# Kernel optimization log

Measured on AMD Instinct MI355X. Metric: run time of the kernel, lower is better.

## Reference

```python
import jax, jax.numpy as jnp
import numpy as np

N = 6144       # number of nodes (adj_list[0].shape[0])
NFEAT = 512    # in_dim
NHID = 256     # hid_dim
NCLASS = 8     # out_dim
ADIM = 128     # attention_dim
EPS = 1e-9


def setup_inputs() -> dict:
    key = jax.random.key(0)
    ks = jax.random.split(key, 16)
    rn = lambda k, s, sc=0.05: (jax.random.normal(k, s, dtype=jnp.float32) * sc)
    return {
        # three dense adjacency matrices (non-negative, largely dense surrogate)
        "adj0": jax.random.uniform(ks[0], (N, N), dtype=jnp.float32),
        "adj1": jax.random.uniform(ks[1], (N, N), dtype=jnp.float32),
        "adj2": jax.random.uniform(ks[2], (N, N), dtype=jnp.float32),
        "features": jax.random.normal(ks[3], (N, NFEAT), dtype=jnp.float32),
        # atten / atten2 / atten3 : Linear(N -> ADIM)
        "Wa1": rn(ks[4], (N, ADIM)), "ba1": jnp.zeros((ADIM,), jnp.float32),
        "Wa2": rn(ks[5], (N, ADIM)), "ba2": jnp.zeros((ADIM,), jnp.float32),
        "Wa3": rn(ks[6], (N, ADIM)), "ba3": jnp.zeros((ADIM,), jnp.float32),
        # agg : Linear(3*ADIM -> 3)
        "Wagg": rn(ks[7], (3 * ADIM, 3)), "bagg": jnp.zeros((3,), jnp.float32),
        # gcn1 : GraphConvolution(NFEAT -> NHID)
        "W1": rn(ks[8], (NFEAT, NHID)), "b1": jnp.zeros((NHID,), jnp.float32),
        # Q/K/V : Linear(NHID -> NHID)
        "Wq": rn(ks[9], (NHID, NHID)), "bq": jnp.zeros((NHID,), jnp.float32),
        "Wk": rn(ks[10], (NHID, NHID)), "bk": jnp.zeros((NHID,), jnp.float32),
        "Wv": rn(ks[11], (NHID, NHID)), "bv": jnp.zeros((NHID,), jnp.float32),
        # gcn2 : GraphConvolution(NHID -> NCLASS)
        "W2": rn(ks[12], (NHID, NCLASS)), "b2": jnp.zeros((NCLASS,), jnp.float32),
    }


def _gcn_norm(a):
    # symmetric normalization D^{-1/2} A D^{-1/2}
    d = jnp.sum(a, axis=1)
    dinv = jnp.where(d > 0, jax.lax.rsqrt(d + EPS), 0.0)
    return dinv[:, None] * a * dinv[None, :]


def reference(adj0, adj1, adj2, features,
              Wa1, ba1, Wa2, ba2, Wa3, ba3, Wagg, bagg,
              W1, b1, Wq, bq, Wk, bk, Wv, bv, W2, b2):
    # adjacency attention weights
    z1 = adj0 @ Wa1 + ba1                      # [N, ADIM]
    z2 = adj1 @ Wa2 + ba2
    z3 = adj2 @ Wa3 + ba3
    z4 = jnp.concatenate((z1, z2, z3), axis=1) @ Wagg + bagg   # [N, 3]
    nz = jax.nn.softmax(z4, axis=1)
    # torch broadcasting: nz[:, i] (shape [N]) scales COLUMNS of adj_i
    adj = nz[:, 0] * adj0 + nz[:, 1] * adj1 + nz[:, 2] * adj2  # [N, N]
    # gcn1
    x = jax.nn.relu(adj @ (features @ W1) + b1)                # [N, NHID]
    Q_h = x @ Wq + bq
    K_h = x @ Wk + bk
    V_h = x @ Wv + bv
    # adjacency-masked dense attention
    A_tilde = adj * (Q_h @ K_h.T)                              # [N, N]
    attention = jax.nn.softmax(A_tilde, axis=1)
    X_tilde = jax.nn.relu(_gcn_norm(attention) @ V_h)          # [N, NHID]
    # gcn2
    z = adj @ (X_tilde @ W2) + b2                              # [N, NCLASS]
    return jax.nn.softmax(z, axis=1), nz
```

## Files before the change

kernel.cpp:

```cpp
#include <hip/hip_runtime.h>

#define NN 6144
#define NF 512
#define NH 256
#define AD 128
#define NC 8

typedef short bf16x8 __attribute__((ext_vector_type(8)));
typedef float f32x4 __attribute__((ext_vector_type(4)));

__device__ __forceinline__ float4 ld4(const float* p) {
    return *reinterpret_cast<const float4*>(p);
}
__device__ __forceinline__ void st4(float* p, float4 v) {
    *reinterpret_cast<float4*>(p) = v;
}

__device__ __forceinline__ f32x4 mfma16(bf16x8 a, bf16x8 b, f32x4 c) {
    return __builtin_amdgcn_mfma_f32_16x16x32_bf16(a, b, c, 0, 0, 0);
}

__device__ __forceinline__ void async_copy16(const void* g, void* lds) {
    __builtin_amdgcn_global_load_lds(
        (const __attribute__((address_space(1))) void*)g,
        (__attribute__((address_space(3))) void*)lds, 16, 0, 0);
}

__device__ __forceinline__ void split1(float f, ushort& h, ushort& l) {
    unsigned u = __float_as_uint(f);
    unsigned hr = (u + 0x7FFFu + ((u >> 16) & 1u)) >> 16;
    float fh = __uint_as_float(hr << 16);
    float fl = f - fh;
    unsigned ul = __float_as_uint(fl);
    unsigned lr = (ul + 0x7FFFu + ((ul >> 16) & 1u)) >> 16;
    h = (ushort)hr; l = (ushort)lr;
}

__global__ __launch_bounds__(256) void k0_prep(
    const float* __restrict__ Wa1, const float* __restrict__ Wa2, const float* __restrict__ Wa3,
    const float* __restrict__ ba1, const float* __restrict__ ba2, const float* __restrict__ ba3,
    const float* __restrict__ Wagg, const float* __restrict__ bagg,
    float* __restrict__ U, float* __restrict__ cvec)
{
    int idx = blockIdx.x * 256 + threadIdx.x;
    if (idx < 3 * NN * 3) {
        int i = idx / (NN * 3);
        int rem = idx - i * (NN * 3);
        int r = rem / 3, j = rem - 3 * (rem / 3);
        const float* Wa = (i == 0) ? Wa1 : ((i == 1) ? Wa2 : Wa3);
        float s = 0.f;
        #pragma unroll 4
        for (int k = 0; k < AD; ++k)
            s += Wa[(size_t)r * AD + k] * Wagg[(i * AD + k) * 3 + j];
        U[idx] = s;
    }
    if (blockIdx.x == 0 && threadIdx.x < 3) {
        int j = threadIdx.x;
        float s = bagg[j];
        const float* bas[3] = {ba1, ba2, ba3};
        for (int i = 0; i < 3; ++i)
            for (int k = 0; k < AD; ++k)
                s += bas[i][k] * Wagg[(i * AD + k) * 3 + j];
        cvec[j] = s;
    }
}

__global__ __launch_bounds__(256) void k1_nz(
    const float* __restrict__ adj0, const float* __restrict__ adj1, const float* __restrict__ adj2,
    const float* __restrict__ U, const float* __restrict__ cvec,
    float* __restrict__ nzT, float* __restrict__ out_nz)
{
    int r0 = blockIdx.x * 4;
    int tid = threadIdx.x;
    float acc[4][3] = {};
    for (int c = tid; c < NN; c += 256) {
        float u[3][3];
        #pragma unroll
        for (int i = 0; i < 3; ++i) {
            u[i][0] = U[((size_t)i * NN + c) * 3 + 0];
            u[i][1] = U[((size_t)i * NN + c) * 3 + 1];
            u[i][2] = U[((size_t)i * NN + c) * 3 + 2];
        }
        #pragma unroll
        for (int rr = 0; rr < 4; ++rr) {
            size_t off = (size_t)(r0 + rr) * NN + c;
            float a0 = adj0[off], a1 = adj1[off], a2 = adj2[off];
            acc[rr][0] += a0 * u[0][0] + a1 * u[1][0] + a2 * u[2][0];
            acc[rr][1] += a0 * u[0][1] + a1 * u[1][1] + a2 * u[2][1];
            acc[rr][2] += a0 * u[0][2] + a1 * u[1][2] + a2 * u[2][2];
        }
    }
    __shared__ float red[256][12];
    #pragma unroll
    for (int rr = 0; rr < 4; ++rr)
        #pragma unroll
        for (int j = 0; j < 3; ++j)
            red[tid][rr * 3 + j] = acc[rr][j];
    __syncthreads();
    for (int s = 128; s > 0; s >>= 1) {
        if (tid < s) {
            #pragma unroll
            for (int q = 0; q < 12; ++q) red[tid][q] += red[tid + s][q];
        }
        __syncthreads();
    }
    if (tid < 4) {
        int r = r0 + tid;
        float z0 = red[0][tid * 3 + 0] + cvec[0];
        float z1 = red[0][tid * 3 + 1] + cvec[1];
        float z2 = red[0][tid * 3 + 2] + cvec[2];
        float m = fmaxf(z0, fmaxf(z1, z2));
        float e0 = __expf(z0 - m), e1 = __expf(z1 - m), e2 = __expf(z2 - m);
        float inv = 1.f / (e0 + e1 + e2);
        e0 *= inv; e1 *= inv; e2 *= inv;
        nzT[0 * NN + r] = e0; nzT[1 * NN + r] = e1; nzT[2 * NN + r] = e2;
        out_nz[(size_t)r * 3 + 0] = e0;
        out_nz[(size_t)r * 3 + 1] = e1;
        out_nz[(size_t)r * 3 + 2] = e2;
    }
}

__global__ __launch_bounds__(256) void k2_adj(
    const float* __restrict__ adj0, const float* __restrict__ adj1, const float* __restrict__ adj2,
    const float* __restrict__ nzT, float* __restrict__ adj)
{
    size_t idx = (size_t)blockIdx.x * 256 + threadIdx.x;
    size_t e = idx * 4;
    int c = (int)(e % NN);
    float4 a0 = ld4(adj0 + e), a1 = ld4(adj1 + e), a2 = ld4(adj2 + e);
    float4 w0 = ld4(nzT + c), w1 = ld4(nzT + NN + c), w2 = ld4(nzT + 2 * NN + c);
    float4 o;
    o.x = w0.x * a0.x + w1.x * a1.x + w2.x * a2.x;
    o.y = w0.y * a0.y + w1.y * a1.y + w2.y * a2.y;
    o.z = w0.z * a0.z + w1.z * a1.z + w2.z * a2.z;
    o.w = w0.w * a0.w + w1.w * a1.w + w2.w * a2.w;
    st4(adj + e, o);
}

#define BM 64
#define BN 64
#define BK 32
#define ASTR 68

__global__ __launch_bounds__(256) void gemm64(
    const float* __restrict__ A, int lda,
    const float* __restrict__ B, int ldb,
    float* __restrict__ C, int ldc,
    int Kdim, const float* __restrict__ bias, int relu)
{
    __shared__ float As[BK * ASTR];
    __shared__ float Bs[BK * BN];
    int tid = threadIdx.x;
    int tm = tid >> 4, tn = tid & 15;
    int rowBase = blockIdx.y * BM, colBase = blockIdx.x * BN;
    float acc[4][4] = {};
    for (int k0 = 0; k0 < Kdim; k0 += BK) {
        #pragma unroll
        for (int it = 0; it < 2; ++it) {
            int lin = it * 256 + tid;
            int am = lin >> 3, ak4 = lin & 7;
            float4 a = ld4(A + (size_t)(rowBase + am) * lda + k0 + ak4 * 4);
            int kk = ak4 * 4;
            As[(kk + 0) * ASTR + am] = a.x;
            As[(kk + 1) * ASTR + am] = a.y;
            As[(kk + 2) * ASTR + am] = a.z;
            As[(kk + 3) * ASTR + am] = a.w;
        }
        #pragma unroll
        for (int it = 0; it < 2; ++it) {
            int lin = it * 256 + tid;
            int bk = lin >> 4, bn4 = lin & 15;
            float4 b = ld4(B + (size_t)(k0 + bk) * ldb + colBase + bn4 * 4);
            st4(&Bs[bk * BN + bn4 * 4], b);
        }
        __syncthreads();
        #pragma unroll
        for (int k = 0; k < BK; ++k) {
            float4 av = *reinterpret_cast<const float4*>(&As[k * ASTR + tm * 4]);
            float4 bv = *reinterpret_cast<const float4*>(&Bs[k * BN + tn * 4]);
            float am_[4] = {av.x, av.y, av.z, av.w};
            float bn_[4] = {bv.x, bv.y, bv.z, bv.w};
            #pragma unroll
            for (int i = 0; i < 4; ++i)
                #pragma unroll
                for (int j = 0; j < 4; ++j)
                    acc[i][j] += am_[i] * bn_[j];
        }
        __syncthreads();
    }
    #pragma unroll
    for (int i = 0; i < 4; ++i) {
        int row = rowBase + tm * 4 + i;
        int col = colBase + tn * 4;
        float4 o = {acc[i][0], acc[i][1], acc[i][2], acc[i][3]};
        if (bias) {
            o.x += bias[col]; o.y += bias[col + 1];
            o.z += bias[col + 2]; o.w += bias[col + 3];
        }
        if (relu) {
            o.x = fmaxf(o.x, 0.f); o.y = fmaxf(o.y, 0.f);
            o.z = fmaxf(o.z, 0.f); o.w = fmaxf(o.w, 0.f);
        }
        st4(C + (size_t)row * ldc + col, o);
    }
}

__global__ __launch_bounds__(256) void cvt_hl(
    const float* __restrict__ in, ushort* __restrict__ hi, ushort* __restrict__ lo)
{
    size_t base = ((size_t)blockIdx.x * 256 + threadIdx.x) * 4;
    float4 v = ld4(in + base);
    ushort4 h, l;
    split1(v.x, h.x, l.x); split1(v.y, h.y, l.y);
    split1(v.z, h.z, l.z); split1(v.w, h.w, l.w);
    *reinterpret_cast<ushort4*>(hi + base) = h;
    *reinterpret_cast<ushort4*>(lo + base) = l;
}

__global__ __launch_bounds__(256) void cvt_t(
    const float* __restrict__ in, int R, int C,
    ushort* __restrict__ outhi, ushort* __restrict__ outlo)
{
    __shared__ float t[32][33];
    int rb = blockIdx.x * 32, cb = blockIdx.y * 32;
    int tid = threadIdx.x;
    int lr = tid >> 3, lc4 = (tid & 7) * 4;
    float4 v = ld4(in + (size_t)(rb + lr) * C + cb + lc4);
    t[lr][lc4 + 0] = v.x; t[lr][lc4 + 1] = v.y;
    t[lr][lc4 + 2] = v.z; t[lr][lc4 + 3] = v.w;
    __syncthreads();
    ushort4 h, l;
    split1(t[lc4 + 0][lr], h.x, l.x);
    split1(t[lc4 + 1][lr], h.y, l.y);
    split1(t[lc4 + 2][lr], h.z, l.z);
    split1(t[lc4 + 3][lr], h.w, l.w);
    size_t o = (size_t)(cb + lr) * R + rb + lc4;
    *reinterpret_cast<ushort4*>(outhi + o) = h;
    *reinterpret_cast<ushort4*>(outlo + o) = l;
}

#define GBM 128
#define GBN 128
#define GBK 32
#define ASTRS 40

__global__ __launch_bounds__(256) void gemm_a32_bsplit(
    const float* __restrict__ A, int lda,
    const ushort* __restrict__ BThi, const ushort* __restrict__ BTlo, int ldbT,
    float* __restrict__ Cpart, int ldc, int Mtotal, int kspan)
{
    int nt = blockIdx.x >> 2;
    int ks = blockIdx.x & 3;
    int rowBase = blockIdx.y * GBM;
    int colBase = nt * GBN;
    int k_begin = ks * kspan;
    int k_end = k_begin + kspan;

    __shared__ ushort Ahi[GBM * ASTRS];
    __shared__ ushort Alo[GBM * ASTRS];
    __shared__ ushort Bhi[GBN * GBK];
    __shared__ ushort Blo[GBN * GBK];

    int tid = threadIdx.x, lane = tid & 63, wave = tid >> 6;
    int wi = wave >> 1, wj = wave & 1;
    int lm = lane & 15, lk = lane >> 4;

    f32x4 acc[4][4] = {};

    for (int k0 = k_begin; k0 < k_end; k0 += GBK) {
        #pragma unroll
        for (int p = 0; p < 2; ++p) {
            int ch = wave * 2 + p;
            int brow = ch * 16 + (lane >> 2);
            size_t goff = ((size_t)(colBase + brow) * ldbT + k0) * 2 + (size_t)(lane & 3) * 16;
            async_copy16((const char*)BThi + goff, (char*)Bhi + ch * 1024);
            async_copy16((const char*)BTlo + goff, (char*)Blo + ch * 1024);
        }
        #pragma unroll
        for (int it = 0; it < 4; ++it) {
            int lin = it * 256 + tid;
            int ar = lin >> 3, as = lin & 7;
            float4 v = ld4(A + (size_t)(rowBase + ar) * lda + k0 + as * 4);
            ushort4 h, l;
            split1(v.x, h.x, l.x); split1(v.y, h.y, l.y);
            split1(v.z, h.z, l.z); split1(v.w, h.w, l.w);
            *reinterpret_cast<ushort4*>(&Ahi[ar * ASTRS + as * 4]) = h;
            *reinterpret_cast<ushort4*>(&Alo[ar * ASTRS + as * 4]) = l;
        }
        __syncthreads();
        bf16x8 af[4], al[4], bh[4], bl[4];
        #pragma unroll
        for (int i = 0; i < 4; ++i) {
            int r = wi * 64 + i * 16 + lm;
            af[i] = *reinterpret_cast<const bf16x8*>(&Ahi[r * ASTRS + lk * 8]);
            al[i] = *reinterpret_cast<const bf16x8*>(&Alo[r * ASTRS + lk * 8]);
        }
        #pragma unroll
        for (int j = 0; j < 4; ++j) {
            int n = wj * 64 + j * 16 + lm;
            bh[j] = *reinterpret_cast<const bf16x8*>(&Bhi[n * GBK + lk * 8]);
            bl[j] = *reinterpret_cast<const bf16x8*>(&Blo[n * GBK + lk * 8]);
        }
        #pragma unroll
        for (int i = 0; i < 4; ++i)
            #pragma unroll
            for (int j = 0; j < 4; ++j) {
                acc[i][j] = mfma16(af[i], bh[j], acc[i][j]);
                acc[i][j] = mfma16(af[i], bl[j], acc[i][j]);
                acc[i][j] = mfma16(al[i], bh[j], acc[i][j]);
            }
        __syncthreads();
    }
    float* Cp = Cpart + (size_t)ks * Mtotal * ldc;
    #pragma unroll
    for (int i = 0; i < 4; ++i)
        #pragma unroll
        for (int j = 0; j < 4; ++j) {
            int row0 = rowBase + wi * 64 + i * 16 + lk * 4;
            int col = colBase + wj * 64 + j * 16 + lm;
            #pragma unroll
            for (int r = 0; r < 4; ++r)
                Cp[(size_t)(row0 + r) * ldc + col] = acc[i][j][r];
        }
}

__global__ __launch_bounds__(256) void reduce4(
    const float* __restrict__ Cpart, const float* __restrict__ bias,
    float* __restrict__ out, int relu)
{
    size_t base = ((size_t)blockIdx.x * 256 + threadIdx.x) * 4;
    const size_t stride = (size_t)NN * NH;
    float4 a = ld4(Cpart + base);
    float4 b = ld4(Cpart + stride + base);
    float4 c = ld4(Cpart + 2 * stride + base);
    float4 d = ld4(Cpart + 3 * stride + base);
    float4 o = {a.x + b.x + c.x + d.x, a.y + b.y + c.y + d.y,
                a.z + b.z + c.z + d.z, a.w + b.w + c.w + d.w};
    if (bias) {
        int col = (int)(base & (NH - 1));
        float4 bb = ld4(bias + col);
        o.x += bb.x; o.y += bb.y; o.z += bb.z; o.w += bb.w;
    }
    if (relu) {
        o.x = fmaxf(o.x, 0.f); o.y = fmaxf(o.y, 0.f);
        o.z = fmaxf(o.z, 0.f); o.w = fmaxf(o.w, 0.f);
    }
    st4(out + base, o);
}

__global__ __launch_bounds__(256) void gemm_qkt(
    const ushort* __restrict__ Qhi, const ushort* __restrict__ Qlo,
    const ushort* __restrict__ Khi, const ushort* __restrict__ Klo,
    float* __restrict__ S)
{
    __shared__ ushort AhiL[128 * 32];
    __shared__ ushort AloL[128 * 32];
    __shared__ ushort BhiL[128 * 32];
    __shared__ ushort BloL[128 * 32];

    int tid = threadIdx.x, lane = tid & 63, wave = tid >> 6;
    int wi = wave >> 1, wj = wave & 1;
    int lm = lane & 15, lk = lane >> 4;
    int rowBase = blockIdx.y * 128, colBase = blockIdx.x * 128;

    f32x4 acc[4][4] = {};

    for (int k0 = 0; k0 < NH; k0 += 32) {
        #pragma unroll
        for (int p = 0; p < 2; ++p) {
            int ch = wave * 2 + p;
            int rr = ch * 16 + (lane >> 2);
            size_t qoff = ((size_t)(rowBase + rr) * NH + k0) * 2 + (size_t)(lane & 3) * 16;
            size_t koff = ((size_t)(colBase + rr) * NH + k0) * 2 + (size_t)(lane & 3) * 16;
            async_copy16((const char*)Qhi + qoff, (char*)AhiL + ch * 1024);
            async_copy16((const char*)Qlo + qoff, (char*)AloL + ch * 1024);
            async_copy16((const char*)Khi + koff, (char*)BhiL + ch * 1024);
            async_copy16((const char*)Klo + koff, (char*)BloL + ch * 1024);
        }
        __syncthreads();
        bf16x8 af[4], al[4], bh[4], bl[4];
        #pragma unroll
        for (int i = 0; i < 4; ++i) {
            int r = wi * 64 + i * 16 + lm;
            af[i] = *reinterpret_cast<const bf16x8*>(&AhiL[r * 32 + lk * 8]);
            al[i] = *reinterpret_cast<const bf16x8*>(&AloL[r * 32 + lk * 8]);
        }
        #pragma unroll
        for (int j = 0; j < 4; ++j) {
            int n = wj * 64 + j * 16 + lm;
            bh[j] = *reinterpret_cast<const bf16x8*>(&BhiL[n * 32 + lk * 8]);
            bl[j] = *reinterpret_cast<const bf16x8*>(&BloL[n * 32 + lk * 8]);
        }
        #pragma unroll
        for (int i = 0; i < 4; ++i)
            #pragma unroll
            for (int j = 0; j < 4; ++j) {
                acc[i][j] = mfma16(af[i], bh[j], acc[i][j]);
                acc[i][j] = mfma16(af[i], bl[j], acc[i][j]);
                acc[i][j] = mfma16(al[i], bh[j], acc[i][j]);
            }
        __syncthreads();
    }
    #pragma unroll
    for (int i = 0; i < 4; ++i)
        #pragma unroll
        for (int j = 0; j < 4; ++j) {
            int row0 = rowBase + wi * 64 + i * 16 + lk * 4;
            int col = colBase + wj * 64 + j * 16 + lm;
            #pragma unroll
            for (int r = 0; r < 4; ++r) {
                size_t off = (size_t)(row0 + r) * NN + col;
                S[off] = S[off] * acc[i][j][r];
            }
        }
}

__global__ __launch_bounds__(256) void k6b_softmax(float* __restrict__ S)
{
    int r = blockIdx.x, tid = threadIdx.x;
    float* row = S + (size_t)r * NN;
    float v[24];
    #pragma unroll
    for (int i = 0; i < 24; ++i) v[i] = row[tid + i * 256];
    float m = v[0];
    #pragma unroll
    for (int i = 1; i < 24; ++i) m = fmaxf(m, v[i]);
    #pragma unroll
    for (int o = 32; o > 0; o >>= 1) m = fmaxf(m, __shfl_xor(m, o));
    __shared__ float redm[4];
    __shared__ float reds[4];
    if ((tid & 63) == 0) redm[tid >> 6] = m;
    __syncthreads();
    m = fmaxf(fmaxf(redm[0], redm[1]), fmaxf(redm[2], redm[3]));
    float s = 0.f;
    #pragma unroll
    for (int i = 0; i < 24; ++i) { v[i] = __expf(v[i] - m); s += v[i]; }
    #pragma unroll
    for (int o = 32; o > 0; o >>= 1) s += __shfl_xor(s, o);
    if ((tid & 63) == 0) reds[tid >> 6] = s;
    __syncthreads();
    s = reds[0] + reds[1] + reds[2] + reds[3];
    float inv = 1.f / s;
    #pragma unroll
    for (int i = 0; i < 24; ++i) row[tid + i * 256] = v[i] * inv;
}

__global__ __launch_bounds__(256) void k6d_Y(
    const float* __restrict__ Xt, const float* __restrict__ W2, float* __restrict__ Y)
{
    int idx = blockIdx.x * 256 + threadIdx.x;
    int r = idx >> 3, j = idx & 7;
    float s = 0.f;
    #pragma unroll 4
    for (int k = 0; k < NH; ++k) s += Xt[(size_t)r * NH + k] * W2[k * 8 + j];
    Y[idx] = s;
}

__global__ __launch_bounds__(256) void k7_out(
    const float* __restrict__ adj0, const float* __restrict__ adj1, const float* __restrict__ adj2,
    const float* __restrict__ nzT, const float* __restrict__ Y,
    const float* __restrict__ b2, float* __restrict__ out)
{
    int r = blockIdx.x, tid = threadIdx.x;
    float acc[8] = {};
    size_t rowOff = (size_t)r * NN;
    for (int c = tid; c < NN; c += 256) {
        float w0 = nzT[c], w1 = nzT[NN + c], w2 = nzT[2 * NN + c];
        float a = w0 * adj0[rowOff + c] + w1 * adj1[rowOff + c] + w2 * adj2[rowOff + c];
        const float* y = Y + (size_t)c * 8;
        float4 y0 = ld4(y), y1 = ld4(y + 4);
        acc[0] += a * y0.x; acc[1] += a * y0.y; acc[2] += a * y0.z; acc[3] += a * y0.w;
        acc[4] += a * y1.x; acc[5] += a * y1.y; acc[6] += a * y1.z; acc[7] += a * y1.w;
    }
    __shared__ float red[256][9];
    #pragma unroll
    for (int j = 0; j < 8; ++j) red[tid][j] = acc[j];
    __syncthreads();
    for (int s2 = 128; s2 > 0; s2 >>= 1) {
        if (tid < s2) {
            #pragma unroll
            for (int j = 0; j < 8; ++j) red[tid][j] += red[tid + s2][j];
        }
        __syncthreads();
    }
    if (tid == 0) {
        float z[8];
        float m = -1e30f;
        #pragma unroll
        for (int j = 0; j < 8; ++j) { z[j] = red[0][j] + b2[j]; m = fmaxf(m, z[j]); }
        float s = 0.f;
        #pragma unroll
        for (int j = 0; j < 8; ++j) { z[j] = __expf(z[j] - m); s += z[j]; }
        float inv = 1.f / s;
        #pragma unroll
        for (int j = 0; j < 8; ++j) out[(size_t)r * NC + j] = z[j] * inv;
    }
}

extern "C" void kernel_launch(void* const* d_in, const int* in_sizes, int n_in,
                              void* d_out, int out_size, void* d_ws, size_t ws_size,
                              hipStream_t stream)
{
    const float* adj0 = (const float*)d_in[0];
    const float* adj1 = (const float*)d_in[1];
    const float* adj2 = (const float*)d_in[2];
    const float* feat = (const float*)d_in[3];
    const float* Wa1 = (const float*)d_in[4];
    const float* ba1 = (const float*)d_in[5];
    const float* Wa2 = (const float*)d_in[6];
    const float* ba2 = (const float*)d_in[7];
    const float* Wa3 = (const float*)d_in[8];
    const float* ba3 = (const float*)d_in[9];
    const float* Wagg = (const float*)d_in[10];
    const float* bagg = (const float*)d_in[11];
    const float* W1 = (const float*)d_in[12];
    const float* b1 = (const float*)d_in[13];
    const float* Wq = (const float*)d_in[14];
    const float* bq = (const float*)d_in[15];
    const float* Wk = (const float*)d_in[16];
    const float* bk = (const float*)d_in[17];
    const float* Wv = (const float*)d_in[18];
    const float* bv = (const float*)d_in[19];
    const float* W2 = (const float*)d_in[20];
    const float* b2 = (const float*)d_in[21];
    float* out = (float*)d_out;
    float* ws = (float*)d_ws;

    const size_t sz_adj = (size_t)NN * NN;
    const size_t sz_m = (size_t)NN * NH;
    float* buf_adj = ws;
    float* nzT     = buf_adj + sz_adj;
    float* U       = nzT + 3 * NN;
    float* cvec    = U + 9 * NN;
    float* fW1     = cvec + 16;
    float* fW1T_hl = fW1 + sz_m;
    float* xbuf    = fW1T_hl + sz_m;
    float* VT_hl   = xbuf + sz_m;
    float* Rbig    = VT_hl + sz_m;
    float* Y       = Rbig + 4 * sz_m;

    ushort* fW1Thi = (ushort*)fW1T_hl;
    ushort* fW1Tlo = fW1Thi + sz_m;
    ushort* VThi = (ushort*)VT_hl;
    ushort* VTlo = VThi + sz_m;
    float* Qm = Rbig;
    float* Km = Rbig + sz_m;
    float* Vm = Rbig + 2 * sz_m;
    ushort* Qhi = (ushort*)fW1;
    ushort* Qlo = Qhi + sz_m;
    ushort* Khi = (ushort*)fW1T_hl;
    ushort* Klo = Khi + sz_m;
    float* Xt = xbuf;

    float* out_nz = out + (size_t)NN * NC;

    k0_prep<<<216, 256, 0, stream>>>(Wa1, Wa2, Wa3, ba1, ba2, ba3, Wagg, bagg, U, cvec);
    k1_nz<<<NN / 4, 256, 0, stream>>>(adj0, adj1, adj2, U, cvec, nzT, out_nz);
    k2_adj<<<(int)(sz_adj / 4 / 256), 256, 0, stream>>>(adj0, adj1, adj2, nzT, buf_adj);
    gemm64<<<dim3(NH / BN, NN / BM), 256, 0, stream>>>(feat, NF, W1, NH, fW1, NH, NF, nullptr, 0);
    cvt_t<<<dim3(NN / 32, NH / 32), 256, 0, stream>>>(fW1, NN, NH, fW1Thi, fW1Tlo);
    gemm_a32_bsplit<<<dim3(2 * 4, NN / GBM), 256, 0, stream>>>(
        buf_adj, NN, fW1Thi, fW1Tlo, NN, Rbig, NH, NN, NN / 4);
    reduce4<<<(int)(sz_m / 4 / 256), 256, 0, stream>>>(Rbig, b1, xbuf, 1);
    gemm64<<<dim3(NH / BN, NN / BM), 256, 0, stream>>>(xbuf, NH, Wq, NH, Qm, NH, NH, bq, 0);
    gemm64<<<dim3(NH / BN, NN / BM), 256, 0, stream>>>(xbuf, NH, Wk, NH, Km, NH, NH, bk, 0);
    gemm64<<<dim3(NH / BN, NN / BM), 256, 0, stream>>>(xbuf, NH, Wv, NH, Vm, NH, NH, bv, 0);
    cvt_hl<<<(int)(sz_m / 4 / 256), 256, 0, stream>>>(Qm, Qhi, Qlo);
    cvt_hl<<<(int)(sz_m / 4 / 256), 256, 0, stream>>>(Km, Khi, Klo);
    cvt_t<<<dim3(NN / 32, NH / 32), 256, 0, stream>>>(Vm, NN, NH, VThi, VTlo);
    gemm_qkt<<<dim3(NN / 128, NN / 128), 256, 0, stream>>>(Qhi, Qlo, Khi, Klo, buf_adj);
    k6b_softmax<<<NN, 256, 0, stream>>>(buf_adj);
    gemm_a32_bsplit<<<dim3(2 * 4, NN / GBM), 256, 0, stream>>>(
        buf_adj, NN, VThi, VTlo, NN, Rbig, NH, NN, NN / 4);
    reduce4<<<(int)(sz_m / 4 / 256), 256, 0, stream>>>(Rbig, nullptr, Xt, 1);
    k6d_Y<<<NN * NC / 256, 256, 0, stream>>>(Xt, W2, Y);
    k7_out<<<NN, 256, 0, stream>>>(adj0, adj1, adj2, nzT, Y, b2, out);
}
```

Baseline: 1.179 ms.

## Fuse row softmax into QK^T epilogue and next GEMM via online max/sum

The separate softmax pass over the 6144x6144 score matrix is removed. gemm_qkt now computes per-tile row max and sum-exp partials, a small merge kernel combines them, and the following GEMM applies exp(x-M)/L while loading A. This saves a full read and write of the NxN matrix. The row-reduction kernels k1_nz and k7_out are also rewritten to one wavefront per row with float4 loads and shuffle reductions instead of LDS tree reductions. The cost is extra exp work inside the GEMM A-load path and partial-stat buffers in the workspace.

```diff
diff --git a/kernel.cpp b/kernel.cpp
--- a/kernel.cpp
+++ b/kernel.cpp
@@ -5,6 +5,7 @@
 #define NH 256
 #define AD 128
 #define NC 8
+#define NCB 48
 
 typedef short bf16x8 __attribute__((ext_vector_type(8)));
 typedef float f32x4 __attribute__((ext_vector_type(4)));
@@ -70,50 +71,44 @@
     const float* __restrict__ U, const float* __restrict__ cvec,
     float* __restrict__ nzT, float* __restrict__ out_nz)
 {
-    int r0 = blockIdx.x * 4;
-    int tid = threadIdx.x;
-    float acc[4][3] = {};
-    for (int c = tid; c < NN; c += 256) {
-        float u[3][3];
+    int wave = threadIdx.x >> 6, lane = threadIdx.x & 63;
+    int r = blockIdx.x * 4 + wave;
+    size_t rowOff = (size_t)r * NN;
+    float acc0 = 0.f, acc1 = 0.f, acc2 = 0.f;
+    for (int c0 = lane * 4; c0 < NN; c0 += 256) {
+        float4 av[3];
+        av[0] = ld4(adj0 + rowOff + c0);
+        av[1] = ld4(adj1 + rowOff + c0);
+        av[2] = ld4(adj2 + rowOff + c0);
         #pragma unroll
         for (int i = 0; i < 3; ++i) {
-            u[i][0] = U[((size_t)i * NN + c) * 3 + 0];
-            u[i][1] = U[((size_t)i * NN + c) * 3 + 1];
-            u[i][2] = U[((size_t)i * NN + c) * 3 + 2];
-        }
-        #pragma unroll
-        for (int rr = 0; rr < 4; ++rr) {
-            size_t off = (size_t)(r0 + rr) * NN + c;
-            float a0 = adj0[off], a1 = adj1[off], a2 = adj2[off];
-            acc[rr][0] += a0 * u[0][0] + a1 * u[1][0] + a2 * u[2][0];
-            acc[rr][1] += a0 * u[0][1] + a1 * u[1][1] + a2 * u[2][1];
-            acc[rr][2] += a0 * u[0][2] + a1 * u[1][2] + a2 * u[2][2];
-        }
-    }
-    __shared__ float red[256][12];
+            const float* Ub = U + ((size_t)i * NN + c0) * 3;
+            float ub[12];
+            *(float4*)&ub[0] = ld4(Ub);
+            *(float4*)&ub[4] = ld4(Ub + 4);
+            *(float4*)&ub[8] = ld4(Ub + 8);
+            float aa[4] = {av[i].x, av[i].y, av[i].z, av[i].w};
+            #pragma unroll
+            for (int k = 0; k < 4; ++k) {
+                acc0 += aa[k] * ub[k * 3 + 0];
+                acc1 += aa[k] * ub[k * 3 + 1];
+                acc2 += aa[k] * ub[k * 3 + 2];
+            }
+        }
+    }
     #pragma unroll
-    for (int rr = 0; rr < 4; ++rr)
-        #pragma unroll
-        for (int j = 0; j < 3; ++j)
-            red[tid][rr * 3 + j] = acc[rr][j];
-    __syncthreads();
-    for (int s = 128; s > 0; s >>= 1) {
-        if (tid < s) {
-            #pragma unroll
-            for (int q = 0; q < 12; ++q) red[tid][q] += red[tid + s][q];
-        }
-        __syncthreads();
-    }
-    if (tid < 4) {
-        int r = r0 + tid;
-        float z0 = red[0][tid * 3 + 0] + cvec[0];
-        float z1 = red[0][tid * 3 + 1] + cvec[1];
-        float z2 = red[0][tid * 3 + 2] + cvec[2];
+    for (int o = 32; o > 0; o >>= 1) {
+        acc0 += __shfl_xor(acc0, o);
+        acc1 += __shfl_xor(acc1, o);
+        acc2 += __shfl_xor(acc2, o);
+    }
+    if (lane == 0) {
+        float z0 = acc0 + cvec[0], z1 = acc1 + cvec[1], z2 = acc2 + cvec[2];
         float m = fmaxf(z0, fmaxf(z1, z2));
         float e0 = __expf(z0 - m), e1 = __expf(z1 - m), e2 = __expf(z2 - m);
         float inv = 1.f / (e0 + e1 + e2);
         e0 *= inv; e1 *= inv; e2 *= inv;
-        nzT[0 * NN + r] = e0; nzT[1 * NN + r] = e1; nzT[2 * NN + r] = e2;
+        nzT[r] = e0; nzT[NN + r] = e1; nzT[2 * NN + r] = e2;
         out_nz[(size_t)r * 3 + 0] = e0;
         out_nz[(size_t)r * 3 + 1] = e1;
         out_nz[(size_t)r * 3 + 2] = e2;
@@ -247,7 +242,8 @@
 __global__ __launch_bounds__(256) void gemm_a32_bsplit(
     const float* __restrict__ A, int lda,
     const ushort* __restrict__ BThi, const ushort* __restrict__ BTlo, int ldbT,
-    float* __restrict__ Cpart, int ldc, int Mtotal, int kspan)
+    float* __restrict__ Cpart, int ldc, int Mtotal, int kspan,
+    const float* __restrict__ rowM, const float* __restrict__ rowInvL)
 {
     int nt = blockIdx.x >> 2;
     int ks = blockIdx.x & 3;
@@ -281,6 +277,14 @@
             int lin = it * 256 + tid;
             int ar = lin >> 3, as = lin & 7;
             float4 v = ld4(A + (size_t)(rowBase + ar) * lda + k0 + as * 4);
+            if (rowM != nullptr) {
+                float M = rowM[rowBase + ar];
+                float s = rowInvL[rowBase + ar];
+                v.x = __expf(v.x - M) * s;
+                v.y = __expf(v.y - M) * s;
+                v.z = __expf(v.z - M) * s;
+                v.w = __expf(v.w - M) * s;
+            }
             ushort4 h, l;
             split1(v.x, h.x, l.x); split1(v.y, h.y, l.y);
             split1(v.z, h.z, l.z); split1(v.w, h.w, l.w);
@@ -351,12 +355,14 @@
 __global__ __launch_bounds__(256) void gemm_qkt(
     const ushort* __restrict__ Qhi, const ushort* __restrict__ Qlo,
     const ushort* __restrict__ Khi, const ushort* __restrict__ Klo,
-    float* __restrict__ S)
+    float* __restrict__ S, float* __restrict__ part_m, float* __restrict__ part_l)
 {
     __shared__ ushort AhiL[128 * 32];
     __shared__ ushort AloL[128 * 32];
     __shared__ ushort BhiL[128 * 32];
     __shared__ ushort BloL[128 * 32];
+    __shared__ float sm[2][2][64];
+    __shared__ float sl[2][2][64];
 
     int tid = threadIdx.x, lane = tid & 63, wave = tid >> 6;
     int wi = wave >> 1, wj = wave & 1;
@@ -410,39 +416,52 @@
             #pragma unroll
             for (int r = 0; r < 4; ++r) {
                 size_t off = (size_t)(row0 + r) * NN + col;
-                S[off] = S[off] * acc[i][j][r];
+                float sv = S[off] * acc[i][j][r];
+                S[off] = sv;
+                acc[i][j][r] = sv;
             }
         }
-}
-
-__global__ __launch_bounds__(256) void k6b_softmax(float* __restrict__ S)
-{
-    int r = blockIdx.x, tid = threadIdx.x;
-    float* row = S + (size_t)r * NN;
-    float v[24];
     #pragma unroll
-    for (int i = 0; i < 24; ++i) v[i] = row[tid + i * 256];
-    float m = v[0];
-    #pragma unroll
-    for (int i = 1; i < 24; ++i) m = fmaxf(m, v[i]);
-    #pragma unroll
-    for (int o = 32; o > 0; o >>= 1) m = fmaxf(m, __shfl_xor(m, o));
-    __shared__ float redm[4];
-    __shared__ float reds[4];
-    if ((tid & 63) == 0) redm[tid >> 6] = m;
+    for (int i = 0; i < 4; ++i)
+        #pragma unroll
+        for (int r = 0; r < 4; ++r) {
+            float m = fmaxf(fmaxf(acc[i][0][r], acc[i][1][r]),
+                            fmaxf(acc[i][2][r], acc[i][3][r]));
+            #pragma unroll
+            for (int o = 1; o < 16; o <<= 1) m = fmaxf(m, __shfl_xor(m, o));
+            float l = 0.f;
+            #pragma unroll
+            for (int j = 0; j < 4; ++j) l += __expf(acc[i][j][r] - m);
+            #pragma unroll
+            for (int o = 1; o < 16; o <<= 1) l += __shfl_xor(l, o);
+            if (lm == 0) {
+                sm[wi][wj][i * 16 + lk * 4 + r] = m;
+                sl[wi][wj][i * 16 + lk * 4 + r] = l;
+            }
+        }
     __syncthreads();
-    m = fmaxf(fmaxf(redm[0], redm[1]), fmaxf(redm[2], redm[3]));
-    float s = 0.f;
-    #pragma unroll
-    for (int i = 0; i < 24; ++i) { v[i] = __expf(v[i] - m); s += v[i]; }
-    #pragma unroll
-    for (int o = 32; o > 0; o >>= 1) s += __shfl_xor(s, o);
-    if ((tid & 63) == 0) reds[tid >> 6] = s;
-    __syncthreads();
-    s = reds[0] + reds[1] + reds[2] + reds[3];
-    float inv = 1.f / s;
-    #pragma unroll
-    for (int i = 0; i < 24; ++i) row[tid + i * 256] = v[i] * inv;
+    if (tid < 128) {
+        int wi2 = tid >> 6, rl = tid & 63;
+        float m0 = sm[wi2][0][rl], m1 = sm[wi2][1][rl];
+        float M = fmaxf(m0, m1);
+        float L = sl[wi2][0][rl] * __expf(m0 - M) + sl[wi2][1][rl] * __expf(m1 - M);
+        part_m[(size_t)blockIdx.x * NN + rowBase + tid] = M;
+        part_l[(size_t)blockIdx.x * NN + rowBase + tid] = L;
+    }
+}
+
+__global__ __launch_bounds__(256) void k_ml_merge(
+    const float* __restrict__ pm, const float* __restrict__ pl,
+    float* __restrict__ rowM, float* __restrict__ rowInvL)
+{
+    int r = blockIdx.x * 256 + threadIdx.x;
+    float M = -1e30f;
+    for (int cb = 0; cb < NCB; ++cb) M = fmaxf(M, pm[(size_t)cb * NN + r]);
+    float L = 0.f;
+    for (int cb = 0; cb < NCB; ++cb)
+        L += pl[(size_t)cb * NN + r] * __expf(pm[(size_t)cb * NN + r] - M);
+    rowM[r] = M;
+    rowInvL[r] = 1.f / L;
 }
 
 __global__ __launch_bounds__(256) void k6d_Y(
@@ -461,33 +480,38 @@
     const float* __restrict__ nzT, const float* __restrict__ Y,
     const float* __restrict__ b2, float* __restrict__ out)
 {
-    int r = blockIdx.x, tid = threadIdx.x;
+    int wave = threadIdx.x >> 6, lane = threadIdx.x & 63;
+    int r = blockIdx.x * 4 + wave;
+    size_t rowOff = (size_t)r * NN;
     float acc[8] = {};
-    size_t rowOff = (size_t)r * NN;
-    for (int c = tid; c < NN; c += 256) {
-        float w0 = nzT[c], w1 = nzT[NN + c], w2 = nzT[2 * NN + c];
-        float a = w0 * adj0[rowOff + c] + w1 * adj1[rowOff + c] + w2 * adj2[rowOff + c];
-        const float* y = Y + (size_t)c * 8;
-        float4 y0 = ld4(y), y1 = ld4(y + 4);
-        acc[0] += a * y0.x; acc[1] += a * y0.y; acc[2] += a * y0.z; acc[3] += a * y0.w;
-        acc[4] += a * y1.x; acc[5] += a * y1.y; acc[6] += a * y1.z; acc[7] += a * y1.w;
-    }
-    __shared__ float red[256][9];
+    for (int c0 = lane * 4; c0 < NN; c0 += 256) {
+        float4 a0 = ld4(adj0 + rowOff + c0);
+        float4 a1 = ld4(adj1 + rowOff + c0);
+        float4 a2 = ld4(adj2 + rowOff + c0);
+        float4 w0 = ld4(nzT + c0), w1 = ld4(nzT + NN + c0), w2 = ld4(nzT + 2 * NN + c0);
+        float a[4] = {w0.x * a0.x + w1.x * a1.x + w2.x * a2.x,
+                      w0.y * a0.y + w1.y * a1.y + w2.y * a2.y,
+                      w0.z * a0.z + w1.z * a1.z + w2.z * a2.z,
+                      w0.w * a0.w + w1.w * a1.w + w2.w * a2.w};
+        #pragma unroll
+        for (int k = 0; k < 4; ++k) {
+            const float* y = Y + (size_t)(c0 + k) * 8;
+            float4 y0 = ld4(y), y1 = ld4(y + 4);
+            acc[0] += a[k] * y0.x; acc[1] += a[k] * y0.y;
+            acc[2] += a[k] * y0.z; acc[3] += a[k] * y0.w;
+            acc[4] += a[k] * y1.x; acc[5] += a[k] * y1.y;
+            acc[6] += a[k] * y1.z; acc[7] += a[k] * y1.w;
+        }
+    }
     #pragma unroll
-    for (int j = 0; j < 8; ++j) red[tid][j] = acc[j];
-    __syncthreads();
-    for (int s2 = 128; s2 > 0; s2 >>= 1) {
-        if (tid < s2) {
-            #pragma unroll
-            for (int j = 0; j < 8; ++j) red[tid][j] += red[tid + s2][j];
-        }
-        __syncthreads();
-    }
-    if (tid == 0) {
+    for (int o = 32; o > 0; o >>= 1)
+        #pragma unroll
+        for (int j = 0; j < 8; ++j) acc[j] += __shfl_xor(acc[j], o);
+    if (lane == 0) {
         float z[8];
         float m = -1e30f;
         #pragma unroll
-        for (int j = 0; j < 8; ++j) { z[j] = red[0][j] + b2[j]; m = fmaxf(m, z[j]); }
+        for (int j = 0; j < 8; ++j) { z[j] = acc[j] + b2[j]; m = fmaxf(m, z[j]); }
         float s = 0.f;
         #pragma unroll
         for (int j = 0; j < 8; ++j) { z[j] = __expf(z[j] - m); s += z[j]; }
@@ -538,6 +562,10 @@
     float* VT_hl   = xbuf + sz_m;
     float* Rbig    = VT_hl + sz_m;
     float* Y       = Rbig + 4 * sz_m;
+    float* part_m  = Y + (size_t)NN * NC;
+    float* part_l  = part_m + (size_t)NCB * NN;
+    float* rowM    = part_l + (size_t)NCB * NN;
+    float* rowInvL = rowM + NN;
 
     ushort* fW1Thi = (ushort*)fW1T_hl;
     ushort* fW1Tlo = fW1Thi + sz_m;
@@ -560,7 +588,7 @@
     gemm64<<<dim3(NH / BN, NN / BM), 256, 0, stream>>>(feat, NF, W1, NH, fW1, NH, NF, nullptr, 0);
     cvt_t<<<dim3(NN / 32, NH / 32), 256, 0, stream>>>(fW1, NN, NH, fW1Thi, fW1Tlo);
     gemm_a32_bsplit<<<dim3(2 * 4, NN / GBM), 256, 0, stream>>>(
-        buf_adj, NN, fW1Thi, fW1Tlo, NN, Rbig, NH, NN, NN / 4);
+        buf_adj, NN, fW1Thi, fW1Tlo, NN, Rbig, NH, NN, NN / 4, nullptr, nullptr);
     reduce4<<<(int)(sz_m / 4 / 256), 256, 0, stream>>>(Rbig, b1, xbuf, 1);
     gemm64<<<dim3(NH / BN, NN / BM), 256, 0, stream>>>(xbuf, NH, Wq, NH, Qm, NH, NH, bq, 0);
     gemm64<<<dim3(NH / BN, NN / BM), 256, 0, stream>>>(xbuf, NH, Wk, NH, Km, NH, NH, bk, 0);
@@ -568,11 +596,12 @@
     cvt_hl<<<(int)(sz_m / 4 / 256), 256, 0, stream>>>(Qm, Qhi, Qlo);
     cvt_hl<<<(int)(sz_m / 4 / 256), 256, 0, stream>>>(Km, Khi, Klo);
     cvt_t<<<dim3(NN / 32, NH / 32), 256, 0, stream>>>(Vm, NN, NH, VThi, VTlo);
-    gemm_qkt<<<dim3(NN / 128, NN / 128), 256, 0, stream>>>(Qhi, Qlo, Khi, Klo, buf_adj);
-    k6b_softmax<<<NN, 256, 0, stream>>>(buf_adj);
+    gemm_qkt<<<dim3(NN / 128, NN / 128), 256, 0, stream>>>(
+        Qhi, Qlo, Khi, Klo, buf_adj, part_m, part_l);
+    k_ml_merge<<<NN / 256, 256, 0, stream>>>(part_m, part_l, rowM, rowInvL);
     gemm_a32_bsplit<<<dim3(2 * 4, NN / GBM), 256, 0, stream>>>(
-        buf_adj, NN, VThi, VTlo, NN, Rbig, NH, NN, NN / 4);
+        buf_adj, NN, VThi, VTlo, NN, Rbig, NH, NN, NN / 4, rowM, rowInvL);
     reduce4<<<(int)(sz_m / 4 / 256), 256, 0, stream>>>(Rbig, nullptr, Xt, 1);
     k6d_Y<<<NN * NC / 256, 256, 0, stream>>>(Xt, W2, Y);
-    k7_out<<<NN, 256, 0, stream>>>(adj0, adj1, adj2, nzT, Y, b2, out);
-}
+    k7_out<<<NN / 4, 256, 0, stream>>>(adj0, adj1, adj2, nzT, Y, b2, out);
+}
```

New measurement: 1.377 ms. +16.8%, slower.
